# Performance work log

Measured on AMD Instinct MI355X. Metric: run time of the kernel, lower is better.

The kernel has to match this reference:

```python
import jax, jax.numpy as jnp
import numpy as np

N, E, D, L = 50000, 400000, 128, 5
NTYPE, NATTR, NDEPTH = 100, 100, 21
BN_EPS = 1e-5


def _bn(z, gamma, beta):
    # training-mode BatchNorm1d over the node axis (biased variance, as torch)
    mu = jnp.mean(z, axis=0)
    var = jnp.mean(jnp.square(z - mu), axis=0)
    return (z - mu) * jax.lax.rsqrt(var + BN_EPS) * gamma + beta


def setup_inputs() -> dict:
    key = jax.random.key(0)
    ks = jax.random.split(key, 20)
    s = 0.05
    inp = {
        "x": jax.random.randint(ks[0], (N, 2), 0, NTYPE),
        "node_depth": jax.random.randint(ks[1], (N,), 0, NDEPTH),
        "edge_index": jax.random.randint(ks[2], (2, E), 0, N),
        "edge_attr": jax.random.normal(ks[3], (E, 2), dtype=jnp.float32),
        # node encoder tables
        "type_emb": jax.random.normal(ks[4], (NTYPE, D)) * s,
        "attr_emb": jax.random.normal(ks[5], (NATTR, D)) * s,
        "depth_emb": jax.random.normal(ks[6], (NDEPTH, D)) * s,
        # per-layer GIN params, stacked over L
        "We": jax.random.normal(ks[7], (L, 2, D)) * s,
        "be": jnp.zeros((L, D)),
        "eps": jnp.zeros((L,)),
        "W1": jax.random.normal(ks[8], (L, D, 2 * D)) * s,
        "b1": jnp.zeros((L, 2 * D)),
        "g1": jnp.ones((L, 2 * D)),
        "bt1": jnp.zeros((L, 2 * D)),
        "W2": jax.random.normal(ks[9], (L, 2 * D, D)) * s,
        "b2": jnp.zeros((L, D)),
        "go": jnp.ones((L, D)),
        "bo": jnp.zeros((L, D)),
    }
    return inp


def reference(x, node_depth, edge_index, edge_attr,
              type_emb, attr_emb, depth_emb,
              We, be, eps, W1, b1, g1, bt1, W2, b2, go, bo):
    # node encoder: type + attr + depth embeddings  -> [N, D]
    h = (type_emb[x[:, 0]] + attr_emb[x[:, 1]]
         + depth_emb[jnp.clip(node_depth, 0, NDEPTH - 1)])
    src, dst = edge_index[0], edge_index[1]
    n = h.shape[0]
    for l in range(L):
        # GINConv: gather -> relu(x_j + edge_emb) -> scatter-add
        edge_emb = edge_attr @ We[l] + be[l]                 # [E, D]
        msg = jax.nn.relu(h[src] + edge_emb)                 # [E, D]
        agg = jax.ops.segment_sum(msg, dst, num_segments=n)  # [N, D]
        z = (1.0 + eps[l]) * h + agg
        # mlp: Linear -> BN -> ReLU -> Linear
        z = _bn(z @ W1[l] + b1[l], g1[l], bt1[l])
        z = jax.nn.relu(z) @ W2[l] + b2[l]
        # outer batchnorm
        z = _bn(z, go[l], bo[l])
        if l < L - 1:  # relu on all but last layer (dropout p=0 -> identity)
            z = jax.nn.relu(z)
        h = z
    return h  # JK='last'
```

## Files before the change

### kernel.cpp

```cpp
#include <hip/hip_runtime.h>
#include <hip/hip_bf16.h>

#define NN  50000
#define NE  400000
#define DD  128
#define DD2 256
#define NL  5
#define NB_SCAN 196
#define GB  256
#define NCH 1563

typedef __hip_bfloat16 bf16;
typedef __attribute__((ext_vector_type(8))) short bf16x8;
typedef __attribute__((ext_vector_type(4))) float f32x4;

__device__ __forceinline__ float b2f(bf16 v) { return __bfloat162float(v); }
__device__ __forceinline__ bool probe_bf(const void* g1) {
    return ((const unsigned*)g1)[0] == 0x3F803F80u;
}
__device__ __forceinline__ float ldp(const void* p, int i, bool bf) {
    return bf ? b2f(((const bf16*)p)[i]) : ((const float*)p)[i];
}
__device__ __forceinline__ void ldp8(const void* p, int i, bool bf, float* o) {
    if (bf) {
        union { int4 v; bf16 b[8]; } u;
        u.v = *(const int4*)((const bf16*)p + i);
#pragma unroll
        for (int j = 0; j < 8; j++) o[j] = b2f(u.b[j]);
    } else {
        float4 a = *(const float4*)((const float*)p + i);
        float4 b = *(const float4*)((const float*)p + i + 4);
        o[0]=a.x; o[1]=a.y; o[2]=a.z; o[3]=a.w;
        o[4]=b.x; o[5]=b.y; o[6]=b.z; o[7]=b.w;
    }
}

__global__ void enc_kernel(const int* __restrict__ x, const int* __restrict__ dep,
                           const void* te, const void* ae, const void* de,
                           const void* probe, float* __restrict__ h,
                           bf16* __restrict__ h2, int h2ok) {
    int t = blockIdx.x * 256 + threadIdx.x;
    if (t >= NN * DD) return;
    bool bf = probe_bf(probe);
    int i = t >> 7, d = t & (DD - 1);
    int dp = dep[i];
    dp = dp < 0 ? 0 : (dp > 20 ? 20 : dp);
    float a = ldp(te, x[2 * i] * DD + d, bf);
    float b = ldp(ae, x[2 * i + 1] * DD + d, bf);
    float c = ldp(de, dp * DD + d, bf);
    float s;
    if (bf) {
        s = b2f(__float2bfloat16(a + b));
        s = b2f(__float2bfloat16(s + c));
    } else {
        s = a + b + c;
    }
    h[t] = s;
    if (h2ok) h2[t] = __float2bfloat16(s);
}

__global__ void hist_kernel(const int* __restrict__ ei, int* __restrict__ cnt) {
    int e = blockIdx.x * 256 + threadIdx.x;
    if (e < NE) atomicAdd(&cnt[ei[NE + e]], 1);
}

__global__ void bsum_kernel(const int* __restrict__ cnt, int* __restrict__ bsum) {
    __shared__ int sm[256];
    int i = blockIdx.x * 256 + threadIdx.x;
    sm[threadIdx.x] = (i < NN) ? cnt[i] : 0;
    __syncthreads();
    for (int s = 128; s > 0; s >>= 1) {
        if (threadIdx.x < s) sm[threadIdx.x] += sm[threadIdx.x + s];
        __syncthreads();
    }
    if (threadIdx.x == 0) bsum[blockIdx.x] = sm[0];
}

__global__ void bscan_kernel(const int* __restrict__ bsum, int* __restrict__ boff, int nb) {
    __shared__ int sm[256];
    int t = threadIdx.x;
    int v = (t < nb) ? bsum[t] : 0;
    sm[t] = v; __syncthreads();
    for (int s = 1; s < 256; s <<= 1) {
        int a = (t >= s) ? sm[t - s] : 0;
        __syncthreads();
        sm[t] += a;
        __syncthreads();
    }
    if (t < nb) boff[t] = sm[t] - v;
}

__global__ void offs_kernel(const int* __restrict__ cnt, const int* __restrict__ boff,
                            int* __restrict__ offs, int* __restrict__ cur) {
    __shared__ int sm[256];
    int t = threadIdx.x;
    int i = blockIdx.x * 256 + t;
    int v = (i < NN) ? cnt[i] : 0;
    sm[t] = v; __syncthreads();
    for (int s = 1; s < 256; s <<= 1) {
        int a = (t >= s) ? sm[t - s] : 0;
        __syncthreads();
        sm[t] += a;
        __syncthreads();
    }
    int excl = sm[t] - v + boff[blockIdx.x];
    if (i < NN) { offs[i] = excl; cur[i] = excl; }
    if (i == NN - 1) offs[NN] = excl + v;
}

__global__ void place_kernel(const int* __restrict__ ei, const float* __restrict__ ea,
                             int* __restrict__ cur, int* __restrict__ srcS,
                             unsigned* __restrict__ eaS) {
    int e = blockIdx.x * 256 + threadIdx.x;
    if (e >= NE) return;
    int dst = ei[NE + e];
    int p = atomicAdd(&cur[dst], 1);
    srcS[p] = ei[e];
    union { bf16 b[2]; unsigned u; } pk;
    pk.b[0] = __float2bfloat16(ea[2 * e]);
    pk.b[1] = __float2bfloat16(ea[2 * e + 1]);
    eaS[p] = pk.u;
}

__global__ void wtrans2_kernel(const void* W1, const void* W2, const void* probe,
                               bf16* __restrict__ W1tH, bf16* __restrict__ W1tL,
                               bf16* __restrict__ W2tH, bf16* __restrict__ W2tL) {
    bool bf = probe_bf(probe);
    int idx = blockIdx.x * 256 + threadIdx.x;
    if (idx >= NL * DD * DD2) return;
    int l = idx / (DD * DD2), rem = idx % (DD * DD2);
    {
        int k = rem / DD2, n = rem % DD2;
        float w = ldp(W1, idx, bf);
        bf16 hb = __float2bfloat16(w);
        size_t o = ((size_t)l * DD2 + n) * DD + k;
        W1tH[o] = hb;
        W1tL[o] = __float2bfloat16(w - b2f(hb));
    }
    {
        int k = rem / DD, n = rem % DD;
        float w = ldp(W2, idx, bf);
        bf16 hb = __float2bfloat16(w);
        size_t o = ((size_t)l * DD + n) * DD2 + k;
        W2tH[o] = hb;
        W2tL[o] = __float2bfloat16(w - b2f(hb));
    }
}

template<int H2>
__global__ __launch_bounds__(256)
void agg_v2(const int* __restrict__ offs, const int* __restrict__ srcS,
            const unsigned* __restrict__ eaS, const void* We, const void* be,
            const void* epsp, const void* probe, const float* __restrict__ h,
            const bf16* __restrict__ h2, float* __restrict__ zpre, int l) {
    bool bf = probe_bf(probe);
    int wave = threadIdx.x >> 6, lane = threadIdx.x & 63;
    int node = blockIdx.x * 4 + wave;
    if (node >= NN) return;
    int d0 = lane * 2;
    float w00 = ldp(We, l * 2 * DD + d0, bf),      w01 = ldp(We, l * 2 * DD + d0 + 1, bf);
    float w10 = ldp(We, l * 2 * DD + DD + d0, bf), w11 = ldp(We, l * 2 * DD + DD + d0 + 1, bf);
    float bb0 = ldp(be, l * DD + d0, bf),          bb1 = ldp(be, l * DD + d0 + 1, bf);
    float cf = 1.0f + ldp(epsp, l, bf);
    int s = offs[node], e = offs[node + 1];
    float acc0 = 0.f, acc1 = 0.f;
    int j = s;
#define AGG_ONE(SRC, EA)                                                        \
    {   float hx, hy;                                                          \
        if (H2) { union { unsigned u; bf16 b[2]; } hv;                         \
                  hv.u = *(const unsigned*)&h2[(size_t)(SRC) * DD + d0];       \
                  hx = b2f(hv.b[0]); hy = b2f(hv.b[1]); }                      \
        else    { float2 hv = *(const float2*)&h[(size_t)(SRC) * DD + d0];     \
                  hx = hv.x; hy = hv.y; }                                      \
        union { unsigned u; bf16 b[2]; } ap; ap.u = (EA);                      \
        float ax = b2f(ap.b[0]), ay = b2f(ap.b[1]);                            \
        acc0 += fmaxf(hx + ax * w00 + ay * w10 + bb0, 0.f);                    \
        acc1 += fmaxf(hy + ax * w01 + ay * w11 + bb1, 0.f); }
    for (; j + 4 <= e; j += 4) {
        int i0 = srcS[j], i1 = srcS[j + 1], i2 = srcS[j + 2], i3 = srcS[j + 3];
        unsigned e0 = eaS[j], e1 = eaS[j + 1], e2 = eaS[j + 2], e3 = eaS[j + 3];
        AGG_ONE(i0, e0) AGG_ONE(i1, e1) AGG_ONE(i2, e2) AGG_ONE(i3, e3)
    }
    for (; j < e; j++) { int i0 = srcS[j]; unsigned e0 = eaS[j]; AGG_ONE(i0, e0) }
#undef AGG_ONE
    float2 hs = *(const float2*)&h[(size_t)node * DD + d0];
    float2 o; o.x = fmaf(cf, hs.x, acc0); o.y = fmaf(cf, hs.y, acc1);
    *(float2*)&zpre[(size_t)node * DD + d0] = o;
}

__global__ __launch_bounds__(512, 2)
void gemm1_v2(const float* __restrict__ zpre, const bf16* __restrict__ W1tH,
              const bf16* __restrict__ W1tL, const void* b1, const void* probe,
              bf16* __restrict__ z1, float* __restrict__ P1s, float* __restrict__ P1q,
              int l) {
    __shared__ float smS[DD2], smQ[DD2];
    bool bf = probe_bf(probe);
    int tid = threadIdx.x;
    int lane = tid & 63, wave = tid >> 6;
    int wq = wave & 3, wr = wave >> 2;
    int ln15 = lane & 15, kg = lane >> 4;

    const bf16* WlH = W1tH + (size_t)l * DD2 * DD;
    const bf16* WlL = W1tL + (size_t)l * DD2 * DD;

    bf16x8 bh[4][4], bl[4][4];
#pragma unroll
    for (int t = 0; t < 4; t++) {
        int n = (wq * 4 + t) * 16 + ln15;
#pragma unroll
        for (int s = 0; s < 4; s++) {
            size_t off = (size_t)n * DD + s * 32 + kg * 8;
            bh[t][s] = *(const bf16x8*)&WlH[off];
            bl[t][s] = *(const bf16x8*)&WlL[off];
        }
    }
    float bias[4];
#pragma unroll
    for (int t = 0; t < 4; t++) bias[t] = ldp(b1, l * DD2 + (wq * 4 + t) * 16 + ln15, bf);

    float sp[4] = {0.f, 0.f, 0.f, 0.f}, qp[4] = {0.f, 0.f, 0.f, 0.f};

    for (int chunk = blockIdx.x; chunk < NCH; chunk += GB) {
        int rowbase = chunk * 32 + wr * 16;
        int arow = rowbase + ln15;
        bool aval = arow < NN;
        f32x4 acc[4];
#pragma unroll
        for (int t = 0; t < 4; t++) acc[t] = (f32x4){0.f, 0.f, 0.f, 0.f};
#pragma unroll
        for (int s = 0; s < 4; s++) {
            float av[8];
            if (aval) {
                float4 p0 = *(const float4*)&zpre[(size_t)arow * DD + s * 32 + kg * 8];
                float4 p1 = *(const float4*)&zpre[(size_t)arow * DD + s * 32 + kg * 8 + 4];
                av[0]=p0.x; av[1]=p0.y; av[2]=p0.z; av[3]=p0.w;
                av[4]=p1.x; av[5]=p1.y; av[6]=p1.z; av[7]=p1.w;
            } else {
#pragma unroll
                for (int j = 0; j < 8; j++) av[j] = 0.f;
            }
            union { bf16x8 v; bf16 e[8]; } ahi, alo;
#pragma unroll
            for (int j = 0; j < 8; j++) {
                bf16 hb = __float2bfloat16(av[j]);
                ahi.e[j] = hb;
                alo.e[j] = __float2bfloat16(av[j] - b2f(hb));
            }
#pragma unroll
            for (int t = 0; t < 4; t++) {
                acc[t] = __builtin_amdgcn_mfma_f32_16x16x32_bf16(ahi.v, bh[t][s], acc[t], 0, 0, 0);
                acc[t] = __builtin_amdgcn_mfma_f32_16x16x32_bf16(alo.v, bh[t][s], acc[t], 0, 0, 0);
                acc[t] = __builtin_amdgcn_mfma_f32_16x16x32_bf16(ahi.v, bl[t][s], acc[t], 0, 0, 0);
            }
        }
#pragma unroll
        for (int t = 0; t < 4; t++) {
            int col = (wq * 4 + t) * 16 + ln15;
#pragma unroll
            for (int r = 0; r < 4; r++) {
                int row = rowbase + kg * 4 + r;
                if (row < NN) {
                    float zv = acc[t][r] + bias[t];
                    bf16 zb = __float2bfloat16(zv);
                    z1[(size_t)row * DD2 + col] = zb;
                    float vv = b2f(zb);
                    sp[t] += vv; qp[t] += vv * vv;
                }
            }
        }
    }
#pragma unroll
    for (int t = 0; t < 4; t++) {
        sp[t] += __shfl_xor(sp[t], 16); sp[t] += __shfl_xor(sp[t], 32);
        qp[t] += __shfl_xor(qp[t], 16); qp[t] += __shfl_xor(qp[t], 32);
    }
    if (tid < DD2) { smS[tid] = 0.f; smQ[tid] = 0.f; }
    __syncthreads();
    if ((lane & 48) == 0) {
#pragma unroll
        for (int t = 0; t < 4; t++) {
            int col = (wq * 4 + t) * 16 + ln15;
            atomicAdd(&smS[col], sp[t]);
            atomicAdd(&smQ[col], qp[t]);
        }
    }
    __syncthreads();
    if (tid < DD2) {
        P1s[(size_t)blockIdx.x * DD2 + tid] = smS[tid];
        P1q[(size_t)blockIdx.x * DD2 + tid] = smQ[tid];
    }
}

__global__ __launch_bounds__(512, 2)
void gemm2_v2(const bf16* __restrict__ z1, const float* __restrict__ s1,
              const float* __restrict__ t1, const bf16* __restrict__ W2tH,
              const bf16* __restrict__ W2tL, const void* b2, const void* probe,
              float* __restrict__ out, float* __restrict__ P2s, float* __restrict__ P2q,
              int l) {
    __shared__ float smS[DD], smQ[DD];
    bool bf = probe_bf(probe);
    int tid = threadIdx.x;
    int lane = tid & 63, wave = tid >> 6;
    int wq = wave & 3, wr = wave >> 2;
    int ln15 = lane & 15, kg = lane >> 4;

    const bf16* WlH = W2tH + (size_t)l * DD * DD2;
    const bf16* WlL = W2tL + (size_t)l * DD * DD2;

    bf16x8 bh[2][8], bl[2][8];
#pragma unroll
    for (int t = 0; t < 2; t++) {
        int n = (wq * 2 + t) * 16 + ln15;
#pragma unroll
        for (int s = 0; s < 8; s++) {
            size_t off = (size_t)n * DD2 + s * 32 + kg * 8;
            bh[t][s] = *(const bf16x8*)&WlH[off];
            bl[t][s] = *(const bf16x8*)&WlL[off];
        }
    }
    float bias[2];
#pragma unroll
    for (int t = 0; t < 2; t++) bias[t] = ldp(b2, l * DD + (wq * 2 + t) * 16 + ln15, bf);

    float sp[2] = {0.f, 0.f}, qp[2] = {0.f, 0.f};

    for (int chunk = blockIdx.x; chunk < NCH; chunk += GB) {
        int rowbase = chunk * 32 + wr * 16;
        int arow = rowbase + ln15;
        bool aval = arow < NN;
        f32x4 acc[2];
        acc[0] = (f32x4){0.f, 0.f, 0.f, 0.f};
        acc[1] = (f32x4){0.f, 0.f, 0.f, 0.f};
#pragma unroll
        for (int s = 0; s < 8; s++) {
            int k0 = s * 32 + kg * 8;
            float az[8];
            if (aval) {
                union { int4 v; bf16 b[8]; } u;
                u.v = *(const int4*)&z1[(size_t)arow * DD2 + k0];
                float4 c0 = *(const float4*)&s1[k0];
                float4 c1 = *(const float4*)&s1[k0 + 4];
                float4 d0 = *(const float4*)&t1[k0];
                float4 d1 = *(const float4*)&t1[k0 + 4];
                float sc[8] = {c0.x,c0.y,c0.z,c0.w,c1.x,c1.y,c1.z,c1.w};
                float tt[8] = {d0.x,d0.y,d0.z,d0.w,d1.x,d1.y,d1.z,d1.w};
#pragma unroll
                for (int j = 0; j < 8; j++)
                    az[j] = fmaxf(fmaf(b2f(u.b[j]), sc[j], tt[j]), 0.f);
            } else {
#pragma unroll
                for (int j = 0; j < 8; j++) az[j] = 0.f;
            }
            union { bf16x8 v; bf16 e[8]; } ahi, alo;
#pragma unroll
            for (int j = 0; j < 8; j++) {
                bf16 hb = __float2bfloat16(az[j]);
                ahi.e[j] = hb;
                alo.e[j] = __float2bfloat16(az[j] - b2f(hb));
            }
#pragma unroll
            for (int t = 0; t < 2; t++) {
                acc[t] = __builtin_amdgcn_mfma_f32_16x16x32_bf16(ahi.v, bh[t][s], acc[t], 0, 0, 0);
                acc[t] = __builtin_amdgcn_mfma_f32_16x16x32_bf16(alo.v, bh[t][s], acc[t], 0, 0, 0);
                acc[t] = __builtin_amdgcn_mfma_f32_16x16x32_bf16(ahi.v, bl[t][s], acc[t], 0, 0, 0);
            }
        }
#pragma unroll
        for (int t = 0; t < 2; t++) {
            int col = (wq * 2 + t) * 16 + ln15;
#pragma unroll
            for (int r = 0; r < 4; r++) {
                int row = rowbase + kg * 4 + r;
                if (row < NN) {
                    float zv = acc[t][r] + bias[t];
                    out[(size_t)row * DD + col] = zv;
                    sp[t] += zv; qp[t] += zv * zv;
                }
            }
        }
    }
#pragma unroll
    for (int t = 0; t < 2; t++) {
        sp[t] += __shfl_xor(sp[t], 16); sp[t] += __shfl_xor(sp[t], 32);
        qp[t] += __shfl_xor(qp[t], 16); qp[t] += __shfl_xor(qp[t], 32);
    }
    if (tid < DD) { smS[tid] = 0.f; smQ[tid] = 0.f; }
    __syncthreads();
    if ((lane & 48) == 0) {
#pragma unroll
        for (int t = 0; t < 2; t++) {
            int col = (wq * 2 + t) * 16 + ln15;
            atomicAdd(&smS[col], sp[t]);
            atomicAdd(&smQ[col], qp[t]);
        }
    }
    __syncthreads();
    if (tid < DD) {
        P2s[(size_t)blockIdx.x * DD + tid] = smS[tid];
        P2q[(size_t)blockIdx.x * DD + tid] = smQ[tid];
    }
}

template<int C>
__global__ void fin_v2(const float* __restrict__ Ps, const float* __restrict__ Pq,
                       const void* gamma, const void* beta, const void* probe,
                       float* __restrict__ s, float* __restrict__ t, int l) {
    int c = threadIdx.x;
    if (c >= C) return;
    bool bf = probe_bf(probe);
    float ssum = 0.f, qsum = 0.f;
    for (int b = 0; b < GB; b++) {
        ssum += Ps[(size_t)b * C + c];
        qsum += Pq[(size_t)b * C + c];
    }
    const float inv = 1.0f / (float)NN;
    float mu = ssum * inv;
    float var = qsum * inv - mu * mu;
    float sc = ldp(gamma, l * C + c, bf) * rsqrtf(var + 1e-5f);
    s[c] = sc;
    t[c] = ldp(beta, l * C + c, bf) - mu * sc;
}

__global__ void bn_apply2(const float* __restrict__ zin, const float* __restrict__ s,
                          const float* __restrict__ t, float* __restrict__ out,
                          bf16* __restrict__ h2, int relu, int h2ok) {
    int i = blockIdx.x * 256 + threadIdx.x;
    if (i >= NN * DD / 4) return;
    int d = (i * 4) & (DD - 1);
    float4 v = ((const float4*)zin)[i];
    float4 sc = *(const float4*)&s[d];
    float4 tt = *(const float4*)&t[d];
    float4 r;
    r.x = fmaf(v.x, sc.x, tt.x);
    r.y = fmaf(v.y, sc.y, tt.y);
    r.z = fmaf(v.z, sc.z, tt.z);
    r.w = fmaf(v.w, sc.w, tt.w);
    if (relu) {
        r.x = fmaxf(r.x, 0.f); r.y = fmaxf(r.y, 0.f);
        r.z = fmaxf(r.z, 0.f); r.w = fmaxf(r.w, 0.f);
    }
    ((float4*)out)[i] = r;
    if (h2ok) {
        union { bf16 b[4]; int2 p; } o;
        o.b[0] = __float2bfloat16(r.x); o.b[1] = __float2bfloat16(r.y);
        o.b[2] = __float2bfloat16(r.z); o.b[3] = __float2bfloat16(r.w);
        *(int2*)&h2[(size_t)i * 4] = o.p;
    }
}

__global__ void scatter_kernel(const int* __restrict__ ei, const float* __restrict__ ea,
                               const void* We, const void* be, const void* probe,
                               const float* __restrict__ h, float* __restrict__ agg,
                               int l, int aok) {
    if (!aok) return;
    bool bf = probe_bf(probe);
    int e = blockIdx.x * 2 + (threadIdx.x >> 7);
    int d = threadIdx.x & (DD - 1);
    int src = ei[e];
    int dst = ei[NE + e];
    float a0 = ea[2 * e], a1 = ea[2 * e + 1];
    float w0 = ldp(We, l * 2 * DD + d, bf);
    float w1 = ldp(We, l * 2 * DD + DD + d, bf);
    float bb = ldp(be, l * DD + d, bf);
    float m = h[src * DD + d] + a0 * w0 + a1 * w1 + bb;
    if (m > 0.0f) atomicAdd(&agg[dst * DD + d], m);
}

__global__ __launch_bounds__(256)
void gemm1_kernel(const float* __restrict__ zin, const float* __restrict__ h,
                  const void* W1, const void* b1, const void* epsp, const void* probe,
                  bf16* __restrict__ z1, int l, int zok) {
    __shared__ float zs[32][36];
    __shared__ float wsh[32][DD2];
    bool bf = probe_bf(probe);
    int tid = threadIdx.x;
    int tx = tid & 31, ty = tid >> 5;
    int row0 = blockIdx.x * 32;
    if (row0 >= NN) return;
    float cf = 1.0f + ldp(epsp, l, bf);
    float acc[4][8];
#pragma unroll
    for (int i = 0; i < 4; i++)
#pragma unroll
        for (int j = 0; j < 8; j++) acc[i][j] = 0.0f;
    int lrow = tid >> 3, lkc = (tid & 7) * 4, wkr = tid >> 5, wcol = (tid & 31) * 8;
    for (int k0 = 0; k0 < DD; k0 += 32) {
        int gr = row0 + lrow;
        float4 zv = make_float4(0.f, 0.f, 0.f, 0.f);
        if (gr < NN) {
            zv = *(const float4*)&zin[gr * DD + k0 + lkc];
            float4 hv = *(const float4*)&h[gr * DD + k0 + lkc];
            zv.x = fmaf(cf, hv.x, zv.x); zv.y = fmaf(cf, hv.y, zv.y);
            zv.z = fmaf(cf, hv.z, zv.z); zv.w = fmaf(cf, hv.w, zv.w);
        }
        *(float4*)&zs[lrow][lkc] = zv;
#pragma unroll
        for (int m = 0; m < 4; m++) {
            int kr = wkr + m * 8;
            float wv[8];
            ldp8(W1, l * DD * DD2 + (k0 + kr) * DD2 + wcol, bf, wv);
            *(float4*)&wsh[kr][wcol]     = make_float4(wv[0], wv[1], wv[2], wv[3]);
            *(float4*)&wsh[kr][wcol + 4] = make_float4(wv[4], wv[5], wv[6], wv[7]);
        }
        __syncthreads();
#pragma unroll 4
        for (int kk = 0; kk < 32; kk++) {
            float zr[4];
#pragma unroll
            for (int i = 0; i < 4; i++) zr[i] = zs[ty * 4 + i][kk];
            float4 w0 = *(float4*)&wsh[kk][tx * 8];
            float4 w1 = *(float4*)&wsh[kk][tx * 8 + 4];
            float wv[8] = {w0.x, w0.y, w0.z, w0.w, w1.x, w1.y, w1.z, w1.w};
#pragma unroll
            for (int i = 0; i < 4; i++)
#pragma unroll
                for (int j = 0; j < 8; j++)
                    acc[i][j] = fmaf(zr[i], wv[j], acc[i][j]);
        }
        __syncthreads();
    }
    float bv[8];
    ldp8(b1, l * DD2 + tx * 8, bf, bv);
#pragma unroll
    for (int i = 0; i < 4; i++) {
        int gr = row0 + ty * 4 + i;
        if (gr < NN && zok) {
            union { int4 v; bf16 b[8]; } o;
#pragma unroll
            for (int j = 0; j < 8; j++) o.b[j] = __float2bfloat16(acc[i][j] + bv[j]);
            *(int4*)&z1[(long)gr * DD2 + tx * 8] = o.v;
        }
    }
}

__global__ __launch_bounds__(256)
void gemm2_kernel(const bf16* __restrict__ z1, const float* __restrict__ s1,
                  const float* __restrict__ t1, const void* W2, const void* b2,
                  const void* probe, float* __restrict__ out, int l, int aok, int zok) {
    __shared__ float zs[32][36];
    __shared__ float wsh[32][DD];
    bool bf = probe_bf(probe);
    int tid = threadIdx.x;
    int tx = tid & 15, ty = tid >> 4;
    int row0 = blockIdx.x * 32;
    if (row0 >= NN) return;
    float acc[2][8];
#pragma unroll
    for (int i = 0; i < 2; i++)
#pragma unroll
        for (int j = 0; j < 8; j++) acc[i][j] = 0.0f;
    int lrow = tid >> 3, lkc = (tid & 7) * 4, wkr = tid >> 4, wcol = (tid & 15) * 8;
    for (int k0 = 0; k0 < DD2; k0 += 32) {
        int gr = row0 + lrow;
        float4 zv = make_float4(0.f, 0.f, 0.f, 0.f);
        if (gr < NN && zok) {
            union { int2 v; bf16 b[4]; } u;
            u.v = *(const int2*)&z1[(long)gr * DD2 + k0 + lkc];
            float4 sc = *(const float4*)&s1[k0 + lkc];
            float4 tt = *(const float4*)&t1[k0 + lkc];
            zv.x = fmaxf(0.f, fmaf(b2f(u.b[0]), sc.x, tt.x));
            zv.y = fmaxf(0.f, fmaf(b2f(u.b[1]), sc.y, tt.y));
            zv.z = fmaxf(0.f, fmaf(b2f(u.b[2]), sc.z, tt.z));
            zv.w = fmaxf(0.f, fmaf(b2f(u.b[3]), sc.w, tt.w));
        }
        *(float4*)&zs[lrow][lkc] = zv;
#pragma unroll
        for (int m = 0; m < 2; m++) {
            int kr = wkr + m * 16;
            float wv[8];
            ldp8(W2, l * DD2 * DD + (k0 + kr) * DD + wcol, bf, wv);
            *(float4*)&wsh[kr][wcol]     = make_float4(wv[0], wv[1], wv[2], wv[3]);
            *(float4*)&wsh[kr][wcol + 4] = make_float4(wv[4], wv[5], wv[6], wv[7]);
        }
        __syncthreads();
#pragma unroll 4
        for (int kk = 0; kk < 32; kk++) {
            float zr[2];
            zr[0] = zs[ty * 2][kk];
            zr[1] = zs[ty * 2 + 1][kk];
            float4 w0 = *(float4*)&wsh[kk][tx * 8];
            float4 w1 = *(float4*)&wsh[kk][tx * 8 + 4];
            float wv[8] = {w0.x, w0.y, w0.z, w0.w, w1.x, w1.y, w1.z, w1.w};
#pragma unroll
            for (int i = 0; i < 2; i++)
#pragma unroll
                for (int j = 0; j < 8; j++)
                    acc[i][j] = fmaf(zr[i], wv[j], acc[i][j]);
        }
        __syncthreads();
    }
    float bv[8];
    ldp8(b2, l * DD + tx * 8, bf, bv);
#pragma unroll
    for (int i = 0; i < 2; i++) {
        int gr = row0 + ty * 2 + i;
        if (gr < NN && aok) {
            float4 o0 = make_float4(acc[i][0] + bv[0], acc[i][1] + bv[1],
                                    acc[i][2] + bv[2], acc[i][3] + bv[3]);
            float4 o1 = make_float4(acc[i][4] + bv[4], acc[i][5] + bv[5],
                                    acc[i][6] + bv[6], acc[i][7] + bv[7]);
            *(float4*)&out[gr * DD + tx * 8] = o0;
            *(float4*)&out[gr * DD + tx * 8 + 4] = o1;
        }
    }
}

__global__ void bn_stats1_kernel(const bf16* __restrict__ z, float* __restrict__ sum,
                                 float* __restrict__ sq, int zok) {
    int col = threadIdx.x;
    int rbase = blockIdx.x * 256;
    int rend = rbase + 256; if (rend > NN) rend = NN;
    float s = 0.0f, q = 0.0f;
    if (zok)
        for (int r = rbase; r < rend; r++) {
            float v = b2f(z[(long)r * DD2 + col]);
            s += v; q += v * v;
        }
    atomicAdd(&sum[col], s);
    atomicAdd(&sq[col], q);
}

__global__ void bn_stats2_kernel(const float* __restrict__ z, float* __restrict__ sum,
                                 float* __restrict__ sq, int aok) {
    int col = threadIdx.x & (DD - 1);
    int roff = threadIdx.x >> 7;
    int rbase = blockIdx.x * 256;
    int rend = rbase + 256; if (rend > NN) rend = NN;
    float s = 0.0f, q = 0.0f;
    if (aok)
        for (int r = rbase + roff; r < rend; r += 2) {
            float v = z[(long)r * DD + col];
            s += v; q += v * v;
        }
    atomicAdd(&sum[col], s);
    atomicAdd(&sq[col], q);
}

template<int C>
__global__ void bn_finalize_kernel(const float* __restrict__ sum, const float* __restrict__ sq,
                                   const void* gamma, const void* beta, const void* probe,
                                   float* __restrict__ s, float* __restrict__ t, int l) {
    int c = threadIdx.x;
    if (c >= C) return;
    bool bf = probe_bf(probe);
    const float inv = 1.0f / (float)NN;
    float mu = sum[c] * inv;
    float var = sq[c] * inv - mu * mu;
    float sc = ldp(gamma, l * C + c, bf) * rsqrtf(var + 1e-5f);
    s[c] = sc;
    t[c] = ldp(beta, l * C + c, bf) - mu * sc;
}

extern "C" void kernel_launch(void* const* d_in, const int* in_sizes, int n_in,
                              void* d_out, int out_size, void* d_ws, size_t ws_size,
                              hipStream_t stream) {
    const int*   x   = (const int*)d_in[0];
    const int*   dep = (const int*)d_in[1];
    const int*   ei  = (const int*)d_in[2];
    const float* ea  = (const float*)d_in[3];
    const void* te  = d_in[4];
    const void* ae  = d_in[5];
    const void* de  = d_in[6];
    const void* We  = d_in[7];
    const void* be  = d_in[8];
    const void* eps = d_in[9];
    const void* W1  = d_in[10];
    const void* b1  = d_in[11];
    const void* g1  = d_in[12];
    const void* bt1 = d_in[13];
    const void* W2  = d_in[14];
    const void* b2  = d_in[15];
    const void* go  = d_in[16];
    const void* bo  = d_in[17];

    float* h  = (float*)d_out;
    float* ws = (float*)d_ws;
    float* sum1 = ws;
    float* sq1  = ws + 256;
    float* sum2 = ws + 512;
    float* sq2  = ws + 640;
    float* s1   = ws + 768;
    float* t1   = ws + 1024;
    float* s2   = ws + 1280;
    float* t2   = ws + 1408;

    float*  P1s  = ws + 2048;
    float*  P1q  = P1s + GB * DD2;
    float*  P2s  = P1q + GB * DD2;
    float*  P2q  = P2s + GB * DD;
    int*    cnt  = (int*)(P2q + GB * DD);
    int*    offs = cnt + 50048;
    int*    cur  = offs + 50048;
    int*    bsum = cur + 50048;
    int*    boff = bsum + 256;
    int*    srcS = boff + 256;
    unsigned* eaS = (unsigned*)(srcS + NE);
    float*  zpreS = (float*)(eaS + NE);
    bf16*   z1S   = (bf16*)(zpreS + (size_t)NN * DD);
    bf16*   W1tH  = z1S + (size_t)NN * DD2;
    bf16*   W1tL  = W1tH + (size_t)NL * DD2 * DD;
    bf16*   W2tH  = W1tL + (size_t)NL * DD2 * DD;
    bf16*   W2tL  = W2tH + (size_t)NL * DD * DD2;
    bf16*   h2    = W2tL + (size_t)NL * DD * DD2;
    size_t need_noh2 = (size_t)((char*)h2 - (char*)d_ws);
    size_t need_full = need_noh2 + (size_t)NN * DD * sizeof(bf16);

    float* zpreF = ws + 2048;
    bf16*  z1F   = (bf16*)(zpreF + (size_t)NN * DD);
    size_t need_a = 2048u * 4 + (size_t)NN * DD * 4;
    size_t need_z = need_a + (size_t)NN * DD2 * 2;

    int mode = ws_size >= need_full ? 2 : (ws_size >= need_noh2 ? 1 : 0);
    int aok = mode || ws_size >= need_a ? 1 : 0;
    int zok = mode || ws_size >= need_z ? 1 : 0;
    float* zpre = mode ? zpreS : zpreF;
    bf16*  z1   = mode ? z1S   : z1F;

    enc_kernel<<<(NN * DD + 255) / 256, 256, 0, stream>>>(x, dep, te, ae, de, g1, h, h2, mode == 2);

    if (mode) {
        hipMemsetAsync(cnt, 0, 50048 * sizeof(int), stream);
        hist_kernel<<<(NE + 255) / 256, 256, 0, stream>>>(ei, cnt);
        bsum_kernel<<<NB_SCAN, 256, 0, stream>>>(cnt, bsum);
        bscan_kernel<<<1, 256, 0, stream>>>(bsum, boff, NB_SCAN);
        offs_kernel<<<NB_SCAN, 256, 0, stream>>>(cnt, boff, offs, cur);
        place_kernel<<<(NE + 255) / 256, 256, 0, stream>>>(ei, ea, cur, srcS, eaS);
        wtrans2_kernel<<<(NL * DD * DD2 + 255) / 256, 256, 0, stream>>>(W1, W2, g1, W1tH, W1tL, W2tH, W2tL);
    }

    for (int l = 0; l < NL; l++) {
        if (mode) {
            if (mode == 2)
                agg_v2<1><<<(NN + 3) / 4, 256, 0, stream>>>(offs, srcS, eaS, We, be, eps, g1, h, h2, zpre, l);
            else
                agg_v2<0><<<(NN + 3) / 4, 256, 0, stream>>>(offs, srcS, eaS, We, be, eps, g1, h, h2, zpre, l);
            gemm1_v2<<<GB, 512, 0, stream>>>(zpre, W1tH, W1tL, b1, g1, z1, P1s, P1q, l);
            fin_v2<DD2><<<1, 256, 0, stream>>>(P1s, P1q, g1, bt1, g1, s1, t1, l);
            gemm2_v2<<<GB, 512, 0, stream>>>(z1, s1, t1, W2tH, W2tL, b2, g1, zpre, P2s, P2q, l);
            fin_v2<DD><<<1, 256, 0, stream>>>(P2s, P2q, go, bo, g1, s2, t2, l);
            bn_apply2<<<(NN * DD / 4 + 255) / 256, 256, 0, stream>>>(
                zpre, s2, t2, h, h2, l < NL - 1 ? 1 : 0, (mode == 2 && l < NL - 1) ? 1 : 0);
        } else {
            hipMemsetAsync(ws, 0, 768 * sizeof(float), stream);
            if (aok) hipMemsetAsync(zpre, 0, (size_t)NN * DD * sizeof(float), stream);
            scatter_kernel<<<NE / 2, 256, 0, stream>>>(ei, ea, We, be, g1, h, zpre, l, aok);
            gemm1_kernel<<<(NN + 31) / 32, 256, 0, stream>>>(zpre, h, W1, b1, eps, g1, z1, l, zok);
            bn_stats1_kernel<<<(NN + 255) / 256, 256, 0, stream>>>(z1, sum1, sq1, zok);
            bn_finalize_kernel<DD2><<<1, DD2, 0, stream>>>(sum1, sq1, g1, bt1, g1, s1, t1, l);
            gemm2_kernel<<<(NN + 31) / 32, 256, 0, stream>>>(z1, s1, t1, W2, b2, g1, zpre, l, aok, zok);
            bn_stats2_kernel<<<(NN + 255) / 256, 256, 0, stream>>>(zpre, sum2, sq2, aok);
            bn_finalize_kernel<DD><<<1, DD, 0, stream>>>(sum2, sq2, go, bo, g1, s2, t2, l);
            bn_apply2<<<(NN * DD / 4 + 255) / 256, 256, 0, stream>>>(
                zpre, s2, t2, h, h2, l < NL - 1 ? 1 : 0, 0);
        }
    }
}
```

Before: 747.2 us.

## Fuse edge aggregation into first GEMM via LDS tiles and parallelize BN finalize

Aggregation now runs inside the first GEMM kernel: each 512-thread block aggregates 16 nodes, writes hi/lo bf16 splits into shared memory, and immediately runs the MFMA GEMM against W1. This removes the fp32 zpre round-trip through global memory and one launch per layer. The second GEMM switches to one 16-row tile per block with 3125 blocks, and the per-block BN partials are stored column-major. They are reduced by one block per channel instead of a single-block serial loop. The cost is that every block reloads its W1/W2 slices from global memory, and the aggregation loop is unrolled to eight edges.

```diff
diff --git a/kernel.cpp b/kernel.cpp
--- a/kernel.cpp
+++ b/kernel.cpp
@@ -7,8 +7,7 @@
 #define DD2 256
 #define NL  5
 #define NB_SCAN 196
-#define GB  256
-#define NCH 1563
+#define NB1 3125
 
 typedef __hip_bfloat16 bf16;
 typedef __attribute__((ext_vector_type(8))) short bf16x8;
@@ -148,24 +147,29 @@
 }
 
 template<int H2>
-__global__ __launch_bounds__(256)
-void agg_v2(const int* __restrict__ offs, const int* __restrict__ srcS,
-            const unsigned* __restrict__ eaS, const void* We, const void* be,
-            const void* epsp, const void* probe, const float* __restrict__ h,
-            const bf16* __restrict__ h2, float* __restrict__ zpre, int l) {
+__global__ __launch_bounds__(512, 4)
+void k1_fused(const int* __restrict__ offs, const int* __restrict__ srcS,
+              const unsigned* __restrict__ eaS, const void* We, const void* be,
+              const void* epsp, const void* probe, const float* __restrict__ h,
+              const bf16* __restrict__ h2, const bf16* __restrict__ W1tH,
+              const bf16* __restrict__ W1tL, const void* b1,
+              bf16* __restrict__ z1, float* __restrict__ P1s, float* __restrict__ P1q,
+              int l) {
+    __shared__ bf16 AH[16][136];
+    __shared__ bf16 AL[16][136];
     bool bf = probe_bf(probe);
-    int wave = threadIdx.x >> 6, lane = threadIdx.x & 63;
-    int node = blockIdx.x * 4 + wave;
-    if (node >= NN) return;
+    int tid = threadIdx.x;
+    int lane = tid & 63, wave = tid >> 6;
+    int ln15 = lane & 15, kg = lane >> 4;
+    int base = blockIdx.x * 16;
+
     int d0 = lane * 2;
     float w00 = ldp(We, l * 2 * DD + d0, bf),      w01 = ldp(We, l * 2 * DD + d0 + 1, bf);
     float w10 = ldp(We, l * 2 * DD + DD + d0, bf), w11 = ldp(We, l * 2 * DD + DD + d0 + 1, bf);
     float bb0 = ldp(be, l * DD + d0, bf),          bb1 = ldp(be, l * DD + d0 + 1, bf);
     float cf = 1.0f + ldp(epsp, l, bf);
-    int s = offs[node], e = offs[node + 1];
-    float acc0 = 0.f, acc1 = 0.f;
-    int j = s;
-#define AGG_ONE(SRC, EA)                                                        \
+
+#define AGG_ONE(SRC, EA, A0, A1)                                               \
     {   float hx, hy;                                                          \
         if (H2) { union { unsigned u; bf16 b[2]; } hv;                         \
                   hv.u = *(const unsigned*)&h2[(size_t)(SRC) * DD + d0];       \
@@ -174,39 +178,47 @@
                   hx = hv.x; hy = hv.y; }                                      \
         union { unsigned u; bf16 b[2]; } ap; ap.u = (EA);                      \
         float ax = b2f(ap.b[0]), ay = b2f(ap.b[1]);                            \
-        acc0 += fmaxf(hx + ax * w00 + ay * w10 + bb0, 0.f);                    \
-        acc1 += fmaxf(hy + ax * w01 + ay * w11 + bb1, 0.f); }
-    for (; j + 4 <= e; j += 4) {
-        int i0 = srcS[j], i1 = srcS[j + 1], i2 = srcS[j + 2], i3 = srcS[j + 3];
-        unsigned e0 = eaS[j], e1 = eaS[j + 1], e2 = eaS[j + 2], e3 = eaS[j + 3];
-        AGG_ONE(i0, e0) AGG_ONE(i1, e1) AGG_ONE(i2, e2) AGG_ONE(i3, e3)
-    }
-    for (; j < e; j++) { int i0 = srcS[j]; unsigned e0 = eaS[j]; AGG_ONE(i0, e0) }
+        A0 += fmaxf(hx + ax * w00 + ay * w10 + bb0, 0.f);                      \
+        A1 += fmaxf(hy + ax * w01 + ay * w11 + bb1, 0.f); }
+
+#pragma unroll
+    for (int nn = 0; nn < 2; nn++) {
+        int node = base + wave * 2 + nn;
+        int s = offs[node], e = offs[node + 1];
+        float a0 = 0.f, a1 = 0.f;
+        int j = s;
+        for (; j + 8 <= e; j += 8) {
+            int i0=srcS[j],i1=srcS[j+1],i2=srcS[j+2],i3=srcS[j+3];
+            int i4=srcS[j+4],i5=srcS[j+5],i6=srcS[j+6],i7=srcS[j+7];
+            unsigned e0=eaS[j],e1=eaS[j+1],e2=eaS[j+2],e3=eaS[j+3];
+            unsigned e4=eaS[j+4],e5=eaS[j+5],e6=eaS[j+6],e7=eaS[j+7];
+            AGG_ONE(i0,e0,a0,a1) AGG_ONE(i1,e1,a0,a1) AGG_ONE(i2,e2,a0,a1) AGG_ONE(i3,e3,a0,a1)
+            AGG_ONE(i4,e4,a0,a1) AGG_ONE(i5,e5,a0,a1) AGG_ONE(i6,e6,a0,a1) AGG_ONE(i7,e7,a0,a1)
+        }
+        for (; j + 2 <= e; j += 2) {
+            int i0=srcS[j], i1=srcS[j+1];
+            unsigned e0=eaS[j], e1=eaS[j+1];
+            AGG_ONE(i0,e0,a0,a1) AGG_ONE(i1,e1,a0,a1)
+        }
+        for (; j < e; j++) { int i0=srcS[j]; unsigned e0=eaS[j]; AGG_ONE(i0,e0,a0,a1) }
+        float2 hs = *(const float2*)&h[(size_t)node * DD + d0];
+        float z0 = fmaf(cf, hs.x, a0), z1v = fmaf(cf, hs.y, a1);
+        bf16 h0 = __float2bfloat16(z0), h1 = __float2bfloat16(z1v);
+        bf16 l0 = __float2bfloat16(z0 - b2f(h0)), l1 = __float2bfloat16(z1v - b2f(h1));
+        int lrow = wave * 2 + nn;
+        union { bf16 b[2]; unsigned u; } ph, pl;
+        ph.b[0] = h0; ph.b[1] = h1; pl.b[0] = l0; pl.b[1] = l1;
+        *(unsigned*)&AH[lrow][d0] = ph.u;
+        *(unsigned*)&AL[lrow][d0] = pl.u;
+    }
 #undef AGG_ONE
-    float2 hs = *(const float2*)&h[(size_t)node * DD + d0];
-    float2 o; o.x = fmaf(cf, hs.x, acc0); o.y = fmaf(cf, hs.y, acc1);
-    *(float2*)&zpre[(size_t)node * DD + d0] = o;
-}
-
-__global__ __launch_bounds__(512, 2)
-void gemm1_v2(const float* __restrict__ zpre, const bf16* __restrict__ W1tH,
-              const bf16* __restrict__ W1tL, const void* b1, const void* probe,
-              bf16* __restrict__ z1, float* __restrict__ P1s, float* __restrict__ P1q,
-              int l) {
-    __shared__ float smS[DD2], smQ[DD2];
-    bool bf = probe_bf(probe);
-    int tid = threadIdx.x;
-    int lane = tid & 63, wave = tid >> 6;
-    int wq = wave & 3, wr = wave >> 2;
-    int ln15 = lane & 15, kg = lane >> 4;
 
     const bf16* WlH = W1tH + (size_t)l * DD2 * DD;
     const bf16* WlL = W1tL + (size_t)l * DD2 * DD;
-
-    bf16x8 bh[4][4], bl[4][4];
-#pragma unroll
-    for (int t = 0; t < 4; t++) {
-        int n = (wq * 4 + t) * 16 + ln15;
+    bf16x8 bh[2][4], bl[2][4];
+#pragma unroll
+    for (int t = 0; t < 2; t++) {
+        int n = (wave * 2 + t) * 16 + ln15;
 #pragma unroll
         for (int s = 0; s < 4; s++) {
             size_t off = (size_t)n * DD + s * 32 + kg * 8;
@@ -214,211 +226,142 @@
             bl[t][s] = *(const bf16x8*)&WlL[off];
         }
     }
-    float bias[4];
-#pragma unroll
-    for (int t = 0; t < 4; t++) bias[t] = ldp(b1, l * DD2 + (wq * 4 + t) * 16 + ln15, bf);
-
-    float sp[4] = {0.f, 0.f, 0.f, 0.f}, qp[4] = {0.f, 0.f, 0.f, 0.f};
-
-    for (int chunk = blockIdx.x; chunk < NCH; chunk += GB) {
-        int rowbase = chunk * 32 + wr * 16;
-        int arow = rowbase + ln15;
-        bool aval = arow < NN;
-        f32x4 acc[4];
-#pragma unroll
-        for (int t = 0; t < 4; t++) acc[t] = (f32x4){0.f, 0.f, 0.f, 0.f};
-#pragma unroll
-        for (int s = 0; s < 4; s++) {
-            float av[8];
-            if (aval) {
-                float4 p0 = *(const float4*)&zpre[(size_t)arow * DD + s * 32 + kg * 8];
-                float4 p1 = *(const float4*)&zpre[(size_t)arow * DD + s * 32 + kg * 8 + 4];
-                av[0]=p0.x; av[1]=p0.y; av[2]=p0.z; av[3]=p0.w;
-                av[4]=p1.x; av[5]=p1.y; av[6]=p1.z; av[7]=p1.w;
-            } else {
-#pragma unroll
-                for (int j = 0; j < 8; j++) av[j] = 0.f;
-            }
-            union { bf16x8 v; bf16 e[8]; } ahi, alo;
-#pragma unroll
-            for (int j = 0; j < 8; j++) {
-                bf16 hb = __float2bfloat16(av[j]);
-                ahi.e[j] = hb;
-                alo.e[j] = __float2bfloat16(av[j] - b2f(hb));
-            }
-#pragma unroll
-            for (int t = 0; t < 4; t++) {
-                acc[t] = __builtin_amdgcn_mfma_f32_16x16x32_bf16(ahi.v, bh[t][s], acc[t], 0, 0, 0);
-                acc[t] = __builtin_amdgcn_mfma_f32_16x16x32_bf16(alo.v, bh[t][s], acc[t], 0, 0, 0);
-                acc[t] = __builtin_amdgcn_mfma_f32_16x16x32_bf16(ahi.v, bl[t][s], acc[t], 0, 0, 0);
-            }
-        }
-#pragma unroll
-        for (int t = 0; t < 4; t++) {
-            int col = (wq * 4 + t) * 16 + ln15;
-#pragma unroll
-            for (int r = 0; r < 4; r++) {
-                int row = rowbase + kg * 4 + r;
-                if (row < NN) {
-                    float zv = acc[t][r] + bias[t];
-                    bf16 zb = __float2bfloat16(zv);
-                    z1[(size_t)row * DD2 + col] = zb;
-                    float vv = b2f(zb);
-                    sp[t] += vv; qp[t] += vv * vv;
-                }
-            }
-        }
-    }
-#pragma unroll
-    for (int t = 0; t < 4; t++) {
-        sp[t] += __shfl_xor(sp[t], 16); sp[t] += __shfl_xor(sp[t], 32);
-        qp[t] += __shfl_xor(qp[t], 16); qp[t] += __shfl_xor(qp[t], 32);
-    }
-    if (tid < DD2) { smS[tid] = 0.f; smQ[tid] = 0.f; }
     __syncthreads();
-    if ((lane & 48) == 0) {
-#pragma unroll
-        for (int t = 0; t < 4; t++) {
-            int col = (wq * 4 + t) * 16 + ln15;
-            atomicAdd(&smS[col], sp[t]);
-            atomicAdd(&smQ[col], qp[t]);
-        }
-    }
-    __syncthreads();
-    if (tid < DD2) {
-        P1s[(size_t)blockIdx.x * DD2 + tid] = smS[tid];
-        P1q[(size_t)blockIdx.x * DD2 + tid] = smQ[tid];
-    }
-}
-
-__global__ __launch_bounds__(512, 2)
-void gemm2_v2(const bf16* __restrict__ z1, const float* __restrict__ s1,
-              const float* __restrict__ t1, const bf16* __restrict__ W2tH,
-              const bf16* __restrict__ W2tL, const void* b2, const void* probe,
-              float* __restrict__ out, float* __restrict__ P2s, float* __restrict__ P2q,
-              int l) {
-    __shared__ float smS[DD], smQ[DD];
+
+    f32x4 acc[2];
+    acc[0] = (f32x4){0.f,0.f,0.f,0.f};
+    acc[1] = (f32x4){0.f,0.f,0.f,0.f};
+#pragma unroll
+    for (int s = 0; s < 4; s++) {
+        bf16x8 ah = *(const bf16x8*)&AH[ln15][s * 32 + kg * 8];
+        bf16x8 al = *(const bf16x8*)&AL[ln15][s * 32 + kg * 8];
+#pragma unroll
+        for (int t = 0; t < 2; t++) {
+            acc[t] = __builtin_amdgcn_mfma_f32_16x16x32_bf16(ah, bh[t][s], acc[t], 0, 0, 0);
+            acc[t] = __builtin_amdgcn_mfma_f32_16x16x32_bf16(al, bh[t][s], acc[t], 0, 0, 0);
+            acc[t] = __builtin_amdgcn_mfma_f32_16x16x32_bf16(ah, bl[t][s], acc[t], 0, 0, 0);
+        }
+    }
+#pragma unroll
+    for (int t = 0; t < 2; t++) {
+        int col = (wave * 2 + t) * 16 + ln15;
+        float bias = ldp(b1, l * DD2 + col, bf);
+        float sp = 0.f, qp = 0.f;
+#pragma unroll
+        for (int r = 0; r < 4; r++) {
+            int row = base + kg * 4 + r;
+            float zv = acc[t][r] + bias;
+            bf16 zb = __float2bfloat16(zv);
+            z1[(size_t)row * DD2 + col] = zb;
+            float vv = b2f(zb);
+            sp += vv; qp += vv * vv;
+        }
+        sp += __shfl_xor(sp, 16); sp += __shfl_xor(sp, 32);
+        qp += __shfl_xor(qp, 16); qp += __shfl_xor(qp, 32);
+        if (lane < 16) {
+            P1s[(size_t)col * NB1 + blockIdx.x] = sp;
+            P1q[(size_t)col * NB1 + blockIdx.x] = qp;
+        }
+    }
+}
+
+__global__ __launch_bounds__(512, 4)
+void k2_gemm(const bf16* __restrict__ z1, const float* __restrict__ s1,
+             const float* __restrict__ t1, const bf16* __restrict__ W2tH,
+             const bf16* __restrict__ W2tL, const void* b2, const void* probe,
+             float* __restrict__ out, float* __restrict__ P2s, float* __restrict__ P2q,
+             int l) {
     bool bf = probe_bf(probe);
     int tid = threadIdx.x;
     int lane = tid & 63, wave = tid >> 6;
-    int wq = wave & 3, wr = wave >> 2;
     int ln15 = lane & 15, kg = lane >> 4;
+    int base = blockIdx.x * 16;
+    int arow = base + ln15;
 
     const bf16* WlH = W2tH + (size_t)l * DD * DD2;
     const bf16* WlL = W2tL + (size_t)l * DD * DD2;
-
-    bf16x8 bh[2][8], bl[2][8];
-#pragma unroll
-    for (int t = 0; t < 2; t++) {
-        int n = (wq * 2 + t) * 16 + ln15;
+    bf16x8 bh[8], bl[8];
+    {
+        int n = wave * 16 + ln15;
 #pragma unroll
         for (int s = 0; s < 8; s++) {
             size_t off = (size_t)n * DD2 + s * 32 + kg * 8;
-            bh[t][s] = *(const bf16x8*)&WlH[off];
-            bl[t][s] = *(const bf16x8*)&WlL[off];
-        }
-    }
-    float bias[2];
-#pragma unroll
-    for (int t = 0; t < 2; t++) bias[t] = ldp(b2, l * DD + (wq * 2 + t) * 16 + ln15, bf);
-
-    float sp[2] = {0.f, 0.f}, qp[2] = {0.f, 0.f};
-
-    for (int chunk = blockIdx.x; chunk < NCH; chunk += GB) {
-        int rowbase = chunk * 32 + wr * 16;
-        int arow = rowbase + ln15;
-        bool aval = arow < NN;
-        f32x4 acc[2];
-        acc[0] = (f32x4){0.f, 0.f, 0.f, 0.f};
-        acc[1] = (f32x4){0.f, 0.f, 0.f, 0.f};
-#pragma unroll
-        for (int s = 0; s < 8; s++) {
-            int k0 = s * 32 + kg * 8;
-            float az[8];
-            if (aval) {
-                union { int4 v; bf16 b[8]; } u;
-                u.v = *(const int4*)&z1[(size_t)arow * DD2 + k0];
-                float4 c0 = *(const float4*)&s1[k0];
-                float4 c1 = *(const float4*)&s1[k0 + 4];
-                float4 d0 = *(const float4*)&t1[k0];
-                float4 d1 = *(const float4*)&t1[k0 + 4];
-                float sc[8] = {c0.x,c0.y,c0.z,c0.w,c1.x,c1.y,c1.z,c1.w};
-                float tt[8] = {d0.x,d0.y,d0.z,d0.w,d1.x,d1.y,d1.z,d1.w};
-#pragma unroll
-                for (int j = 0; j < 8; j++)
-                    az[j] = fmaxf(fmaf(b2f(u.b[j]), sc[j], tt[j]), 0.f);
-            } else {
-#pragma unroll
-                for (int j = 0; j < 8; j++) az[j] = 0.f;
-            }
-            union { bf16x8 v; bf16 e[8]; } ahi, alo;
-#pragma unroll
-            for (int j = 0; j < 8; j++) {
-                bf16 hb = __float2bfloat16(az[j]);
-                ahi.e[j] = hb;
-                alo.e[j] = __float2bfloat16(az[j] - b2f(hb));
-            }
-#pragma unroll
-            for (int t = 0; t < 2; t++) {
-                acc[t] = __builtin_amdgcn_mfma_f32_16x16x32_bf16(ahi.v, bh[t][s], acc[t], 0, 0, 0);
-                acc[t] = __builtin_amdgcn_mfma_f32_16x16x32_bf16(alo.v, bh[t][s], acc[t], 0, 0, 0);
-                acc[t] = __builtin_amdgcn_mfma_f32_16x16x32_bf16(ahi.v, bl[t][s], acc[t], 0, 0, 0);
-            }
-        }
-#pragma unroll
-        for (int t = 0; t < 2; t++) {
-            int col = (wq * 2 + t) * 16 + ln15;
-#pragma unroll
-            for (int r = 0; r < 4; r++) {
-                int row = rowbase + kg * 4 + r;
-                if (row < NN) {
-                    float zv = acc[t][r] + bias[t];
-                    out[(size_t)row * DD + col] = zv;
-                    sp[t] += zv; qp[t] += zv * zv;
-                }
-            }
-        }
-    }
-#pragma unroll
-    for (int t = 0; t < 2; t++) {
-        sp[t] += __shfl_xor(sp[t], 16); sp[t] += __shfl_xor(sp[t], 32);
-        qp[t] += __shfl_xor(qp[t], 16); qp[t] += __shfl_xor(qp[t], 32);
-    }
-    if (tid < DD) { smS[tid] = 0.f; smQ[tid] = 0.f; }
+            bh[s] = *(const bf16x8*)&WlH[off];
+            bl[s] = *(const bf16x8*)&WlL[off];
+        }
+    }
+
+    f32x4 acc = (f32x4){0.f, 0.f, 0.f, 0.f};
+#pragma unroll
+    for (int s = 0; s < 8; s++) {
+        int k0 = s * 32 + kg * 8;
+        union { int4 v; bf16 b[8]; } u;
+        u.v = *(const int4*)&z1[(size_t)arow * DD2 + k0];
+        float4 c0 = *(const float4*)&s1[k0];
+        float4 c1 = *(const float4*)&s1[k0 + 4];
+        float4 d0 = *(const float4*)&t1[k0];
+        float4 d1 = *(const float4*)&t1[k0 + 4];
+        float sc[8] = {c0.x,c0.y,c0.z,c0.w,c1.x,c1.y,c1.z,c1.w};
+        float tt[8] = {d0.x,d0.y,d0.z,d0.w,d1.x,d1.y,d1.z,d1.w};
+        union { bf16x8 v; bf16 e[8]; } ahi, alo;
+#pragma unroll
+        for (int j = 0; j < 8; j++) {
+            float az = fmaxf(fmaf(b2f(u.b[j]), sc[j], tt[j]), 0.f);
+            bf16 hb = __float2bfloat16(az);
+            ahi.e[j] = hb;
+            alo.e[j] = __float2bfloat16(az - b2f(hb));
+        }
+        acc = __builtin_amdgcn_mfma_f32_16x16x32_bf16(ahi.v, bh[s], acc, 0, 0, 0);
+        acc = __builtin_amdgcn_mfma_f32_16x16x32_bf16(alo.v, bh[s], acc, 0, 0, 0);
+        acc = __builtin_amdgcn_mfma_f32_16x16x32_bf16(ahi.v, bl[s], acc, 0, 0, 0);
+    }
+    int col = wave * 16 + ln15;
+    float bias = ldp(b2, l * DD + col, bf);
+    float sp = 0.f, qp = 0.f;
+#pragma unroll
+    for (int r = 0; r < 4; r++) {
+        int row = base + kg * 4 + r;
+        float zv = acc[r] + bias;
+        out[(size_t)row * DD + col] = zv;
+        sp += zv; qp += zv * zv;
+    }
+    sp += __shfl_xor(sp, 16); sp += __shfl_xor(sp, 32);
+    qp += __shfl_xor(qp, 16); qp += __shfl_xor(qp, 32);
+    if (lane < 16) {
+        P2s[(size_t)col * NB1 + blockIdx.x] = sp;
+        P2q[(size_t)col * NB1 + blockIdx.x] = qp;
+    }
+}
+
+template<int C>
+__global__ void fin_v3(const float* __restrict__ Ps, const float* __restrict__ Pq,
+                       int nb, const void* gamma, const void* beta, const void* probe,
+                       float* __restrict__ s, float* __restrict__ t, int l) {
+    __shared__ float rs[256], rq[256];
+    int c = blockIdx.x;
+    float ss = 0.f, qq = 0.f;
+    for (int b = threadIdx.x; b < nb; b += 256) {
+        ss += Ps[(size_t)c * nb + b];
+        qq += Pq[(size_t)c * nb + b];
+    }
+    rs[threadIdx.x] = ss; rq[threadIdx.x] = qq;
     __syncthreads();
-    if ((lane & 48) == 0) {
-#pragma unroll
-        for (int t = 0; t < 2; t++) {
-            int col = (wq * 2 + t) * 16 + ln15;
-            atomicAdd(&smS[col], sp[t]);
-            atomicAdd(&smQ[col], qp[t]);
-        }
-    }
-    __syncthreads();
-    if (tid < DD) {
-        P2s[(size_t)blockIdx.x * DD + tid] = smS[tid];
-        P2q[(size_t)blockIdx.x * DD + tid] = smQ[tid];
-    }
-}
-
-template<int C>
-__global__ void fin_v2(const float* __restrict__ Ps, const float* __restrict__ Pq,
-                       const void* gamma, const void* beta, const void* probe,
-                       float* __restrict__ s, float* __restrict__ t, int l) {
-    int c = threadIdx.x;
-    if (c >= C) return;
-    bool bf = probe_bf(probe);
-    float ssum = 0.f, qsum = 0.f;
-    for (int b = 0; b < GB; b++) {
-        ssum += Ps[(size_t)b * C + c];
-        qsum += Pq[(size_t)b * C + c];
-    }
-    const float inv = 1.0f / (float)NN;
-    float mu = ssum * inv;
-    float var = qsum * inv - mu * mu;
-    float sc = ldp(gamma, l * C + c, bf) * rsqrtf(var + 1e-5f);
-    s[c] = sc;
-    t[c] = ldp(beta, l * C + c, bf) - mu * sc;
+    for (int k = 128; k > 0; k >>= 1) {
+        if (threadIdx.x < k) {
+            rs[threadIdx.x] += rs[threadIdx.x + k];
+            rq[threadIdx.x] += rq[threadIdx.x + k];
+        }
+        __syncthreads();
+    }
+    if (threadIdx.x == 0) {
+        bool bf = probe_bf(probe);
+        const float inv = 1.0f / (float)NN;
+        float mu = rs[0] * inv;
+        float var = rq[0] * inv - mu * mu;
+        float sc = ldp(gamma, l * C + c, bf) * rsqrtf(var + 1e-5f);
+        s[c] = sc;
+        t[c] = ldp(beta, l * C + c, bf) - mu * sc;
+    }
 }
 
 __global__ void bn_apply2(const float* __restrict__ zin, const float* __restrict__ s,
@@ -685,23 +628,23 @@
     float* t2   = ws + 1408;
 
     float*  P1s  = ws + 2048;
-    float*  P1q  = P1s + GB * DD2;
-    float*  P2s  = P1q + GB * DD2;
-    float*  P2q  = P2s + GB * DD;
-    int*    cnt  = (int*)(P2q + GB * DD);
+    float*  P1q  = P1s + (size_t)DD2 * NB1;
+    float*  P2s  = P1q + (size_t)DD2 * NB1;
+    float*  P2q  = P2s + (size_t)DD * NB1;
+    int*    cnt  = (int*)(P2q + (size_t)DD * NB1);
     int*    offs = cnt + 50048;
     int*    cur  = offs + 50048;
     int*    bsum = cur + 50048;
     int*    boff = bsum + 256;
     int*    srcS = boff + 256;
     unsigned* eaS = (unsigned*)(srcS + NE);
-    float*  zpreS = (float*)(eaS + NE);
-    bf16*   z1S   = (bf16*)(zpreS + (size_t)NN * DD);
-    bf16*   W1tH  = z1S + (size_t)NN * DD2;
-    bf16*   W1tL  = W1tH + (size_t)NL * DD2 * DD;
-    bf16*   W2tH  = W1tL + (size_t)NL * DD2 * DD;
-    bf16*   W2tL  = W2tH + (size_t)NL * DD * DD2;
-    bf16*   h2    = W2tL + (size_t)NL * DD * DD2;
+    float*  zout = (float*)(eaS + NE);
+    bf16*   z1S  = (bf16*)(zout + (size_t)NN * DD);
+    bf16*   W1tH = z1S + (size_t)NN * DD2;
+    bf16*   W1tL = W1tH + (size_t)NL * DD2 * DD;
+    bf16*   W2tH = W1tL + (size_t)NL * DD2 * DD;
+    bf16*   W2tL = W2tH + (size_t)NL * DD * DD2;
+    bf16*   h2   = W2tL + (size_t)NL * DD * DD2;
     size_t need_noh2 = (size_t)((char*)h2 - (char*)d_ws);
     size_t need_full = need_noh2 + (size_t)NN * DD * sizeof(bf16);
 
@@ -713,8 +656,7 @@
     int mode = ws_size >= need_full ? 2 : (ws_size >= need_noh2 ? 1 : 0);
     int aok = mode || ws_size >= need_a ? 1 : 0;
     int zok = mode || ws_size >= need_z ? 1 : 0;
-    float* zpre = mode ? zpreS : zpreF;
-    bf16*  z1   = mode ? z1S   : z1F;
+    bf16* z1 = mode ? z1S : z1F;
 
     enc_kernel<<<(NN * DD + 255) / 256, 256, 0, stream>>>(x, dep, te, ae, de, g1, h, h2, mode == 2);
 
@@ -731,27 +673,28 @@
     for (int l = 0; l < NL; l++) {
         if (mode) {
             if (mode == 2)
-                agg_v2<1><<<(NN + 3) / 4, 256, 0, stream>>>(offs, srcS, eaS, We, be, eps, g1, h, h2, zpre, l);
+                k1_fused<1><<<NB1, 512, 0, stream>>>(offs, srcS, eaS, We, be, eps, g1, h, h2,
+                                                     W1tH, W1tL, b1, z1, P1s, P1q, l);
             else
-                agg_v2<0><<<(NN + 3) / 4, 256, 0, stream>>>(offs, srcS, eaS, We, be, eps, g1, h, h2, zpre, l);
-            gemm1_v2<<<GB, 512, 0, stream>>>(zpre, W1tH, W1tL, b1, g1, z1, P1s, P1q, l);
-            fin_v2<DD2><<<1, 256, 0, stream>>>(P1s, P1q, g1, bt1, g1, s1, t1, l);
-            gemm2_v2<<<GB, 512, 0, stream>>>(z1, s1, t1, W2tH, W2tL, b2, g1, zpre, P2s, P2q, l);
-            fin_v2<DD><<<1, 256, 0, stream>>>(P2s, P2q, go, bo, g1, s2, t2, l);
+                k1_fused<0><<<NB1, 512, 0, stream>>>(offs, srcS, eaS, We, be, eps, g1, h, h2,
+                                                     W1tH, W1tL, b1, z1, P1s, P1q, l);
+            fin_v3<DD2><<<DD2, 256, 0, stream>>>(P1s, P1q, NB1, g1, bt1, g1, s1, t1, l);
+            k2_gemm<<<NB1, 512, 0, stream>>>(z1, s1, t1, W2tH, W2tL, b2, g1, zout, P2s, P2q, l);
+            fin_v3<DD><<<DD, 256, 0, stream>>>(P2s, P2q, NB1, go, bo, g1, s2, t2, l);
             bn_apply2<<<(NN * DD / 4 + 255) / 256, 256, 0, stream>>>(
-                zpre, s2, t2, h, h2, l < NL - 1 ? 1 : 0, (mode == 2 && l < NL - 1) ? 1 : 0);
+                zout, s2, t2, h, h2, l < NL - 1 ? 1 : 0, (mode == 2 && l < NL - 1) ? 1 : 0);
         } else {
             hipMemsetAsync(ws, 0, 768 * sizeof(float), stream);
-            if (aok) hipMemsetAsync(zpre, 0, (size_t)NN * DD * sizeof(float), stream);
-            scatter_kernel<<<NE / 2, 256, 0, stream>>>(ei, ea, We, be, g1, h, zpre, l, aok);
-            gemm1_kernel<<<(NN + 31) / 32, 256, 0, stream>>>(zpre, h, W1, b1, eps, g1, z1, l, zok);
+            if (aok) hipMemsetAsync(zpreF, 0, (size_t)NN * DD * sizeof(float), stream);
+            scatter_kernel<<<NE / 2, 256, 0, stream>>>(ei, ea, We, be, g1, h, zpreF, l, aok);
+            gemm1_kernel<<<(NN + 31) / 32, 256, 0, stream>>>(zpreF, h, W1, b1, eps, g1, z1, l, zok);
             bn_stats1_kernel<<<(NN + 255) / 256, 256, 0, stream>>>(z1, sum1, sq1, zok);
             bn_finalize_kernel<DD2><<<1, DD2, 0, stream>>>(sum1, sq1, g1, bt1, g1, s1, t1, l);
-            gemm2_kernel<<<(NN + 31) / 32, 256, 0, stream>>>(z1, s1, t1, W2, b2, g1, zpre, l, aok, zok);
-            bn_stats2_kernel<<<(NN + 255) / 256, 256, 0, stream>>>(zpre, sum2, sq2, aok);
+            gemm2_kernel<<<(NN + 31) / 32, 256, 0, stream>>>(z1, s1, t1, W2, b2, g1, zpreF, l, aok, zok);
+            bn_stats2_kernel<<<(NN + 255) / 256, 256, 0, stream>>>(zpreF, sum2, sq2, aok);
             bn_finalize_kernel<DD><<<1, DD, 0, stream>>>(sum2, sq2, go, bo, g1, s2, t2, l);
             bn_apply2<<<(NN * DD / 4 + 255) / 256, 256, 0, stream>>>(
-                zpre, s2, t2, h, h2, l < NL - 1 ? 1 : 0, 0);
-        }
-    }
-}
+                zpreF, s2, t2, h, h2, l < NL - 1 ? 1 : 0, 0);
+        }
+    }
+}
```

Result: slower. 1.123 ms (+50.3%).
